# Optimization experiments

Hardware: AMD Instinct MI355X
Metric: run time of the kernel (lower is better)

Reference implementation:

```python
import jax, jax.numpy as jnp
import numpy as np

N, E, G = 10000, 80000, 64
F_IN, D, EA, H = 14, 64, 4, 128


def setup_inputs() -> dict:
    key = jax.random.key(0)
    ks = jax.random.split(key, 16)
    f32 = jnp.float32
    def nrm(k, shape, s=0.1):
        return jax.random.normal(k, shape, f32) * s
    return {
        "x": jax.random.normal(ks[0], (N, F_IN), f32),
        "edge_index": jax.random.randint(ks[1], (2, E), 0, N),
        "edge_attr": jax.random.uniform(ks[2], (E, EA), f32),
        "batch": jnp.sort(jax.random.randint(ks[3], (N,), 0, G)),
        "do_dropout": 0,
        "lin0_w": nrm(ks[4], (F_IN, D)), "lin0_b": jnp.zeros((D,), f32),
        "h1_w": nrm(ks[5], (EA, H)), "h1_b": jnp.zeros((H,), f32),
        "h2_w": nrm(ks[6], (H, D * D), 0.02), "h2_b": jnp.zeros((D * D,), f32),
        "conv_root": nrm(ks[7], (D, D)), "conv_bias": jnp.zeros((D,), f32),
        "gru_w_ih": nrm(ks[8], (3 * D, D)), "gru_w_hh": nrm(ks[9], (3 * D, D)),
        "gru_b_ih": jnp.zeros((3 * D,), f32), "gru_b_hh": jnp.zeros((3 * D,), f32),
        "lstm_w_ih": nrm(ks[10], (4 * D, 2 * D)), "lstm_w_hh": nrm(ks[11], (4 * D, D)),
        "lstm_b_ih": jnp.zeros((4 * D,), f32), "lstm_b_hh": jnp.zeros((4 * D,), f32),
        "lin1_w": nrm(ks[12], (2 * D, D)), "lin1_b": jnp.zeros((D,), f32),
        "lin2_w": nrm(ks[13], (D, 1)), "lin2_b": jnp.zeros((1,), f32),
    }


def _seg_softmax(e, seg, n):
    m = jax.ops.segment_max(e, seg, num_segments=n)
    ex = jnp.exp(e - m[seg])
    s = jax.ops.segment_sum(ex, seg, num_segments=n)
    return ex / s[seg]


def _forward(x, edge_index, edge_attr, batch,
             lin0_w, lin0_b, h1_w, h1_b, h2_w, h2_b, conv_root, conv_bias,
             gru_w_ih, gru_w_hh, gru_b_ih, gru_b_hh,
             lstm_w_ih, lstm_w_hh, lstm_b_ih, lstm_b_hh,
             lin1_w, lin1_b, lin2_w, lin2_b):
    src, tgt = edge_index[0], edge_index[1]
    out = jax.nn.relu(x @ lin0_w + lin0_b)              # [N, D]
    h = out
    # edge-conditioned weights: MLP(edge_attr) -> [E, D, D]
    W_e = (jax.nn.relu(edge_attr @ h1_w + h1_b) @ h2_w + h2_b).reshape(E, D, D)
    deg = jax.ops.segment_sum(jnp.ones((E,), out.dtype), tgt, num_segments=N)
    deg = jnp.maximum(deg, 1.0)[:, None]
    for _ in range(3):
        msg = jnp.einsum("ei,eio->eo", out[src], W_e)   # per-edge matmul
        agg = jax.ops.segment_sum(msg, tgt, num_segments=N) / deg  # mean aggr
        m = jax.nn.relu(agg + out @ conv_root + conv_bias)
        # single GRU step (torch nn.GRU, 1 layer, seq_len=1)
        gi = m @ gru_w_ih.T + gru_b_ih
        gh = h @ gru_w_hh.T + gru_b_hh
        ir, iz, in_ = jnp.split(gi, 3, axis=-1)
        hr, hz, hn = jnp.split(gh, 3, axis=-1)
        r = jax.nn.sigmoid(ir + hr)
        z = jax.nn.sigmoid(iz + hz)
        n = jnp.tanh(in_ + r * hn)
        h = (1.0 - z) * n + z * h
        out = h
    # Set2Set pooling, 3 processing steps
    q_star = jnp.zeros((G, 2 * D), out.dtype)
    hs = jnp.zeros((G, D), out.dtype)
    cs = jnp.zeros((G, D), out.dtype)
    for _ in range(3):
        gates = q_star @ lstm_w_ih.T + lstm_b_ih + hs @ lstm_w_hh.T + lstm_b_hh
        i, f, g, o = jnp.split(gates, 4, axis=-1)
        cs = jax.nn.sigmoid(f) * cs + jax.nn.sigmoid(i) * jnp.tanh(g)
        hs = jax.nn.sigmoid(o) * jnp.tanh(cs)
        q = hs                                          # [G, D]
        e = jnp.sum(out * q[batch], axis=-1)            # [N]
        a = _seg_softmax(e, batch, G)
        r = jax.ops.segment_sum(a[:, None] * out, batch, num_segments=G)
        q_star = jnp.concatenate([q, r], axis=-1)
    y = jax.nn.relu(q_star @ lin1_w + lin1_b)
    # do_dropout=False in this reference (eval mode): dropout is identity
    y = y @ lin2_w + lin2_b
    return y.reshape(-1)


def reference(x, edge_index, edge_attr, batch, do_dropout,
              lin0_w, lin0_b, h1_w, h1_b, h2_w, h2_b, conv_root, conv_bias,
              gru_w_ih, gru_w_hh, gru_b_ih, gru_b_hh,
              lstm_w_ih, lstm_w_hh, lstm_b_ih, lstm_b_hh,
              lin1_w, lin1_b, lin2_w, lin2_b):
    return _forward(x, edge_index, edge_attr, batch,
                    lin0_w, lin0_b, h1_w, h1_b, h2_w, h2_b, conv_root, conv_bias,
                    gru_w_ih, gru_w_hh, gru_b_ih, gru_b_hh,
                    lstm_w_ih, lstm_w_hh, lstm_b_ih, lstm_b_hh,
                    lin1_w, lin1_b, lin2_w, lin2_b)
```

## Files before the change

kernel.cpp:

```cpp
#include <hip/hip_runtime.h>
#include <math.h>

#define N_NODES 10000
#define N_EDGES 80000
#define N_GRAPH 64
#define DD 64
#define HIDW 128
#define F_IN 14
#define EAD 4

typedef _Float16 f16x8 __attribute__((ext_vector_type(8)));
typedef float f32x4 __attribute__((ext_vector_type(4)));

__device__ __forceinline__ float sigmoidf_(float x){ return 1.0f/(1.0f+expf(-x)); }

__global__ __launch_bounds__(256) void k_prep_misc(
    const float* __restrict__ h2w, _Float16* __restrict__ Bp,
    const float* __restrict__ gih, const float* __restrict__ ghh,
    const float* __restrict__ lih, const float* __restrict__ lhh,
    float* __restrict__ WihT, float* __restrict__ WhhT,
    float* __restrict__ IhT,  float* __restrict__ HhT,
    const int* __restrict__ tgt, int* __restrict__ cnt,
    const int* __restrict__ batch, int* __restrict__ goff,
    const float* __restrict__ x, const float* __restrict__ l0w,
    const float* __restrict__ l0b, float* __restrict__ s)
{
  int idx = blockIdx.x*256 + threadIdx.x;
  if (idx < 524288){
    int j = idx & 7, l = (idx >> 3) & 63, cg = (idx >> 9) & 3, st = idx >> 11;
    int k = st*32 + ((l >> 4) << 3) + j;
    int h = k >> 6, i = k & 63, o = cg*16 + (l & 15);
    Bp[idx] = (_Float16)h2w[(size_t)h*4096 + i*64 + o];
    return;
  }
  idx -= 524288;
  if (idx < 12288){ int k=idx/192, j=idx%192; WihT[idx]=gih[j*64+k]; return; }
  idx -= 12288;
  if (idx < 12288){ int k=idx/192, j=idx%192; WhhT[idx]=ghh[j*64+k]; return; }
  idx -= 12288;
  if (idx < 32768){ int k=idx>>8, j=idx&255; IhT[idx]=lih[j*128+k]; return; }
  idx -= 32768;
  if (idx < 16384){ int k=idx>>8, j=idx&255; HhT[idx]=lhh[j*64+k]; return; }
  idx -= 16384;
  if (idx < N_EDGES){ atomicAdd(&cnt[tgt[idx]], 1); return; }
  idx -= N_EDGES;
  if (idx < 65){
    int g = idx, lo = 0, hi = N_NODES;
    while (lo < hi){ int mid = (lo+hi)>>1; if (batch[mid] < g) lo = mid+1; else hi = mid; }
    goff[g] = lo; return;
  }
  idx -= 65;
  if (idx < N_NODES*64){
    int n = idx >> 6, o = idx & 63;
    float acc = l0b[o];
    #pragma unroll
    for (int k=0;k<F_IN;++k) acc += x[n*F_IN + k]*l0w[k*64 + o];
    s[idx] = fmaxf(acc, 0.f);
    return;
  }
}
#define PREP_TOT (524288 + 12288 + 12288 + 32768 + 16384 + N_EDGES + 65 + N_NODES*64)


__global__ __launch_bounds__(1024) void k_scan(const int* __restrict__ cnt, int* __restrict__ offs,
                                               int* __restrict__ cursor, float* __restrict__ deg){
  __shared__ int sc[1024];
  int t = threadIdx.x;
  int base = t*10;
  int loc[10]; int tot = 0;
  #pragma unroll
  for (int j=0;j<10;++j){
    int i = base+j;
    int c = (i < N_NODES) ? cnt[i] : 0;
    loc[j] = tot; tot += c;
  }
  sc[t] = tot; __syncthreads();
  for (int st=1; st<1024; st<<=1){
    int v = (t>=st) ? sc[t-st] : 0;
    __syncthreads();
    sc[t] += v;
    __syncthreads();
  }
  int ex = sc[t] - tot;
  #pragma unroll
  for (int j=0;j<10;++j){
    int i = base+j;
    if (i < N_NODES){
      int o = ex + loc[j];
      offs[i] = o; cursor[i] = o;
      int c = cnt[i];
      deg[i] = (float)(c > 0 ? c : 1);
    }
  }
  if (t == 1023) offs[N_NODES] = sc[1023];
}

__global__ void k_sortE(const int* __restrict__ tgt, const int* __restrict__ src,
                        int* __restrict__ cursor, int* __restrict__ srcS, int* __restrict__ pos){
  int e = blockIdx.x*256 + threadIdx.x;
  if (e < N_EDGES){
    int p = atomicAdd(&cursor[tgt[e]], 1);
    srcS[p] = src[e];
    pos[e] = p;
  }
}

__global__ __launch_bounds__(256) void k_hid(const float* __restrict__ ea,
    const float* __restrict__ h1_w, const float* __restrict__ h1_b,
    const int* __restrict__ pos, _Float16* __restrict__ hidS){
  int tid = threadIdx.x;
  int g = tid >> 7, j = tid & 127;
  __shared__ float eL[2][EAD];
  __shared__ int pL[2];
  if (tid < 8){ int gg = tid>>2, k = tid&3; eL[gg][k] = ea[(blockIdx.x*2+gg)*EAD + k]; }
  if (tid < 2) pL[tid] = pos[blockIdx.x*2 + tid];
  __syncthreads();
  float v = h1_b[j];
  #pragma unroll
  for (int k=0;k<EAD;++k) v += eL[g][k]*h1_w[k*HIDW + j];
  hidS[(size_t)pL[g]*HIDW + j] = (_Float16)fmaxf(v, 0.f);
}

__global__ __launch_bounds__(256) void k_aggpre(
    const float* __restrict__ s, const _Float16* __restrict__ hidS,
    const int* __restrict__ offs, const int* __restrict__ srcS,
    _Float16* __restrict__ P, float* __restrict__ Ssum){
  int t = blockIdx.x;
  int tid = threadIdx.x;
  int i8 = tid & 7, hb = tid >> 3;
  __shared__ float sL[8][64];
  __shared__ float hidT[8][128];
  float acc[4][8];
  #pragma unroll
  for (int r=0;r<4;++r)
    #pragma unroll
    for (int ii=0;ii<8;++ii) acc[r][ii] = 0.f;
  float ss[8];
  #pragma unroll
  for (int ii=0;ii<8;++ii) ss[ii] = 0.f;
  int e0 = offs[t], e1 = offs[t+1];
  for (int base = e0; base < e1; base += 8){
    int ecnt = min(8, e1 - base);
    __syncthreads();
    for (int a = tid; a < ecnt*64; a += 256){
      int j = a >> 6, ii = a & 63;
      sL[j][ii] = s[(size_t)srcS[base+j]*64 + ii];
    }
    for (int a = tid; a < ecnt*128; a += 256){
      int j = a >> 7, hh = a & 127;
      hidT[j][(hh & 3)*32 + (hh >> 2)] = (float)hidS[(size_t)(base+j)*HIDW + hh];
    }
    __syncthreads();
    for (int j=0;j<ecnt;++j){
      float hv[4], sv[8];
      #pragma unroll
      for (int r=0;r<4;++r) hv[r] = hidT[j][r*32 + hb];
      #pragma unroll
      for (int ii=0;ii<8;++ii) sv[ii] = sL[j][i8*8 + ii];
      #pragma unroll
      for (int r=0;r<4;++r)
        #pragma unroll
        for (int ii=0;ii<8;++ii) acc[r][ii] += hv[r]*sv[ii];
      if (hb == 0){
        #pragma unroll
        for (int ii=0;ii<8;++ii) ss[ii] += sv[ii];
      }
    }
  }
  _Float16* row = P + (size_t)t*8192;
  #pragma unroll
  for (int r=0;r<4;++r){
    f16x8 pk;
    #pragma unroll
    for (int ii=0;ii<8;++ii) pk[ii] = (_Float16)acc[r][ii];
    *(f16x8*)(row + (hb*4 + r)*64 + i8*8) = pk;
  }
  if (hb == 0){
    float4 v0 = make_float4(ss[0],ss[1],ss[2],ss[3]);
    float4 v1 = make_float4(ss[4],ss[5],ss[6],ss[7]);
    *(float4*)(Ssum + (size_t)t*64 + i8*8)     = v0;
    *(float4*)(Ssum + (size_t)t*64 + i8*8 + 4) = v1;
  }
}

__global__ __launch_bounds__(256) void k_gemm_fused(
    const _Float16* __restrict__ A, const _Float16* __restrict__ Bp,
    const float* __restrict__ Ssum, const float* __restrict__ h2b,
    const float* __restrict__ deg, float* __restrict__ s,
    const float* __restrict__ conv_root, const float* __restrict__ conv_bias,
    const float* __restrict__ WihT, const float* __restrict__ WhhT,
    const float* __restrict__ bih, const float* __restrict__ bhh)
{
  __shared__ _Float16 tile[2][16*1024];
  __shared__ float aggL[16][68];
  __shared__ float hS[16][64];
  __shared__ float xS[16][68];
  int tid = threadIdx.x;
  int t0 = blockIdx.x*16;
  const size_t rowB = (size_t)8192*2;
  int sub = tid >> 7, colb = (tid & 127)*16;
  const char* Ab = (const char*)A + (size_t)t0*rowB;
  f16x8 rg[8];
  int cg = tid >> 6, lane = tid & 63;
  int row = lane & 15, kb = lane >> 4;
  int swz = (row & 7) << 4;
  f32x4 acc = {0.f,0.f,0.f,0.f};

  #pragma unroll
  for (int i2=0;i2<8;++i2){
    int r = i2*2 + sub;
    rg[i2] = *(const f16x8*)(Ab + (size_t)r*rowB + (size_t)(colb ^ ((r&7)<<4)));
  }
  #pragma unroll
  for (int i2=0;i2<8;++i2){
    int r = i2*2 + sub;
    *(f16x8*)((char*)tile[0] + r*2048 + colb) = rg[i2];
  }
  for (int y = 0; y < 8; ++y){
    if (y < 7){
      #pragma unroll
      for (int i2=0;i2<8;++i2){
        int r = i2*2 + sub;
        rg[i2] = *(const f16x8*)(Ab + (size_t)r*rowB + (size_t)(y+1)*2048 + (size_t)(colb ^ ((r&7)<<4)));
      }
    }
    __syncthreads();
    const char* tb = (const char*)tile[y&1] + row*2048;
    int fr0 = y*128;
    #pragma unroll 8
    for (int st = 0; st < 32; ++st){
      f16x8 af = *(const f16x8*)(tb + ((st*64 + kb*16) ^ swz));
      f16x8 bf = *(const f16x8*)(Bp + ((size_t)(fr0 + st*4 + cg)*64 + lane)*8);
      acc = __builtin_amdgcn_mfma_f32_16x16x32_f16(af, bf, acc, 0, 0, 0);
    }
    if (y < 7){
      #pragma unroll
      for (int i2=0;i2<8;++i2){
        int r = i2*2 + sub;
        *(f16x8*)((char*)tile[(y+1)&1] + r*2048 + colb) = rg[i2];
      }
    }
  }
  #pragma unroll
  for (int r=0;r<4;++r) aggL[kb*4 + r][cg*16 + row] = acc[r];
  for (int a = tid; a < 1024; a += 256){
    int nn = a >> 6, o = a & 63;
    hS[nn][o] = s[(size_t)(t0+nn)*64 + o];
    xS[nn][o] = Ssum[(size_t)(t0+nn)*64 + o];
  }
  __syncthreads();
  int o = tid & 63, ng = tid >> 6;
  float aM[4];
  #pragma unroll
  for (int u=0;u<4;++u) aM[u] = aggL[ng + 4*u][o];
  for (int k=0;k<64;++k){
    float w2 = h2b[k*64 + o];
    #pragma unroll
    for (int u=0;u<4;++u) aM[u] += xS[ng + 4*u][k]*w2;
  }
  #pragma unroll
  for (int u=0;u<4;++u) aM[u] = aM[u]/deg[t0 + ng + 4*u] + conv_bias[o];
  for (int k=0;k<64;++k){
    float cr = conv_root[k*64 + o];
    #pragma unroll
    for (int u=0;u<4;++u) aM[u] += hS[ng + 4*u][k]*cr;
  }
  float mM[4];
  #pragma unroll
  for (int u=0;u<4;++u) mM[u] = fmaxf(aM[u], 0.f);
  __syncthreads();
  #pragma unroll
  for (int u=0;u<4;++u) xS[ng + 4*u][o] = mM[u];
  __syncthreads();
  float gi0[4], gi1[4], gi2[4], gh0[4], gh1[4], gh2[4];
  #pragma unroll
  for (int u=0;u<4;++u){
    gi0[u] = bih[o];     gh0[u] = bhh[o];
    gi1[u] = bih[64+o];  gh1[u] = bhh[64+o];
    gi2[u] = bih[128+o]; gh2[u] = bhh[128+o];
  }
  for (int k=0;k<64;++k){
    float wi0 = WihT[k*192 + o], wi1 = WihT[k*192 + 64 + o], wi2 = WihT[k*192 + 128 + o];
    float wh0 = WhhT[k*192 + o], wh1 = WhhT[k*192 + 64 + o], wh2 = WhhT[k*192 + 128 + o];
    #pragma unroll
    for (int u=0;u<4;++u){
      float mk = xS[ng + 4*u][k], hk = hS[ng + 4*u][k];
      gi0[u] += mk*wi0; gh0[u] += hk*wh0;
      gi1[u] += mk*wi1; gh1[u] += hk*wh1;
      gi2[u] += mk*wi2; gh2[u] += hk*wh2;
    }
  }
  #pragma unroll
  for (int u=0;u<4;++u){
    int nn = ng + 4*u;
    float r = sigmoidf_(gi0[u] + gh0[u]);
    float z = sigmoidf_(gi1[u] + gh1[u]);
    float nv = tanhf(gi2[u] + r*gh2[u]);
    float hnew = (1.f - z)*nv + z*hS[nn][o];
    s[(size_t)(t0+nn)*64 + o] = hnew;
  }
}


__global__ __launch_bounds__(256) void k_s2s_all(const float* __restrict__ sND,
    const int* __restrict__ goff,
    const float* __restrict__ IhT, const float* __restrict__ HhT,
    const float* __restrict__ bih, const float* __restrict__ bhh,
    float* __restrict__ ebuf,
    const float* __restrict__ lin1_w, const float* __restrict__ lin1_b,
    const float* __restrict__ lin2_w, const float* __restrict__ lin2_b,
    float* __restrict__ out)
{
  const int CAP = 256;
  __shared__ float sG[256][68];
  __shared__ float eL[256];
  __shared__ float qL[128], hL[64], cL[64], gate[256];
  __shared__ float red[4], redw[4], red2[4][64];
  int g = blockIdx.x, tid = threadIdx.x;
  int w = tid >> 6, lane = tid & 63;
  int n0 = goff[g], n1 = goff[g+1], cnt = n1 - n0;
  int ncap = cnt < CAP ? cnt : CAP;
  for (int idx = tid; idx < ncap*64; idx += 256)
    sG[idx>>6][idx&63] = sND[(size_t)(n0 + (idx>>6))*64 + (idx&63)];
  if (tid < 128) qL[tid] = 0.f;
  if (tid < 64){ hL[tid] = 0.f; cL[tid] = 0.f; }
  __syncthreads();
  for (int step = 0; step < 3; ++step){
    float acc = bih[tid] + bhh[tid];
    #pragma unroll 8
    for (int k=0;k<128;++k) acc += qL[k]*IhT[k*256 + tid];
    #pragma unroll 8
    for (int k=0;k<64;++k)  acc += hL[k]*HhT[k*256 + tid];
    gate[tid] = acc;
    __syncthreads();
    if (tid < 64){
      float i = sigmoidf_(gate[tid]);
      float f = sigmoidf_(gate[64+tid]);
      float gg = tanhf(gate[128+tid]);
      float o = sigmoidf_(gate[192+tid]);
      float cc = f*cL[tid] + i*gg;
      hL[tid] = o*tanhf(cc);
      cL[tid] = cc;
    }
    __syncthreads();
    float wmax = -INFINITY;
    for (int r = w; r < cnt; r += 4){
      float v = (r < CAP) ? sG[r][lane] : sND[(size_t)(n0+r)*64 + lane];
      float p = v * hL[lane];
      #pragma unroll
      for (int s2=32; s2>0; s2>>=1) p += __shfl_xor(p, s2, 64);
      if (lane == 0){ if (r < CAP) eL[r] = p; else ebuf[n0+r] = p; }
      wmax = fmaxf(wmax, p);
    }
    if (lane == 0) red[w] = wmax;
    __syncthreads();
    float m = fmaxf(fmaxf(red[0], red[1]), fmaxf(red[2], red[3]));
    float racc = 0.f, ws = 0.f;
    for (int r = w; r < cnt; r += 4){
      float e = (r < CAP) ? eL[r] : ebuf[n0+r];
      float a = expf(e - m);
      float v = (r < CAP) ? sG[r][lane] : sND[(size_t)(n0+r)*64 + lane];
      racc += a * v;
      ws += a;
    }
    red2[w][lane] = racc;
    if (lane == 0) redw[w] = ws;
    __syncthreads();
    if (tid < 64){
      float rs = red2[0][lane]+red2[1][lane]+red2[2][lane]+red2[3][lane];
      float st = redw[0]+redw[1]+redw[2]+redw[3];
      float rr = (st > 0.f) ? rs/st : 0.f;
      qL[lane] = hL[lane];
      qL[64+lane] = rr;
    }
    __syncthreads();
  }
  {
    float facc = 0.f;
    for (int k = w*32; k < w*32+32; ++k) facc += qL[k]*lin1_w[k*64 + lane];
    red2[w][lane] = facc;
  }
  __syncthreads();
  if (tid < 64){
    float z = fmaxf(lin1_b[lane] + red2[0][lane]+red2[1][lane]+red2[2][lane]+red2[3][lane], 0.f);
    float p = z * lin2_w[lane];
    #pragma unroll
    for (int s2=32; s2>0; s2>>=1) p += __shfl_xor(p, s2, 64);
    if (lane == 0) out[g] = p + lin2_b[0];
  }
}


static inline size_t alignup(size_t x){ return (x + 255) & ~(size_t)255; }

extern "C" void kernel_launch(void* const* d_in, const int* in_sizes, int n_in,
                              void* d_out, int out_size, void* d_ws, size_t ws_size,
                              hipStream_t stream){
  const float* x      = (const float*)d_in[0];
  const int*   ei     = (const int*)  d_in[1];
  const float* ea     = (const float*)d_in[2];
  const int*   batch  = (const int*)  d_in[3];
  const float* lin0_w = (const float*)d_in[5];
  const float* lin0_b = (const float*)d_in[6];
  const float* h1_w   = (const float*)d_in[7];
  const float* h1_b   = (const float*)d_in[8];
  const float* h2_w   = (const float*)d_in[9];
  const float* h2_b   = (const float*)d_in[10];
  const float* conv_root = (const float*)d_in[11];
  const float* conv_bias = (const float*)d_in[12];
  const float* gru_w_ih  = (const float*)d_in[13];
  const float* gru_w_hh  = (const float*)d_in[14];
  const float* gru_b_ih  = (const float*)d_in[15];
  const float* gru_b_hh  = (const float*)d_in[16];
  const float* lstm_w_ih = (const float*)d_in[17];
  const float* lstm_w_hh = (const float*)d_in[18];
  const float* lstm_b_ih = (const float*)d_in[19];
  const float* lstm_b_hh = (const float*)d_in[20];
  const float* lin1_w = (const float*)d_in[21];
  const float* lin1_b = (const float*)d_in[22];
  const float* lin2_w = (const float*)d_in[23];
  const float* lin2_b = (const float*)d_in[24];
  (void)in_sizes; (void)n_in; (void)out_size; (void)ws_size;

  const int* srcA = ei;
  const int* tgtA = ei + N_EDGES;

  char* p = (char*)d_ws;
  size_t off = 0;
  auto take = [&](size_t bytes)->char*{ char* q = p + off; off = alignup(off + bytes); return q; };
  _Float16* Bpack = (_Float16*)take((size_t)524288*2);
  float* sbuf     = (float*)take((size_t)N_NODES*DD*4);
  float* Ssum     = (float*)take((size_t)N_NODES*DD*4);
  _Float16* hidS  = (_Float16*)take((size_t)N_EDGES*HIDW*2);
  float* WihT    = (float*)take(12288*4);
  float* WhhT    = (float*)take(12288*4);
  float* IhT     = (float*)take(32768*4);
  float* HhT     = (float*)take(16384*4);
  float* deg     = (float*)take(N_NODES*4);
  int*   cnt     = (int*)  take(N_NODES*4);
  int*   offs    = (int*)  take((N_NODES+1)*4);
  int*   cursor  = (int*)  take(N_NODES*4);
  int*   srcS    = (int*)  take(N_EDGES*4);
  int*   pos     = (int*)  take(N_EDGES*4);
  int*   goff    = (int*)  take(65*4);
  float* ebuf    = (float*)take(N_NODES*4);
  _Float16* Pbuf = (_Float16*)take((size_t)N_NODES*8192*2);

  hipMemsetAsync(cnt, 0, N_NODES*4, stream);

  k_prep_misc<<<(PREP_TOT + 255)/256, 256, 0, stream>>>(
      h2_w, Bpack, gru_w_ih, gru_w_hh, lstm_w_ih, lstm_w_hh,
      WihT, WhhT, IhT, HhT, tgtA, cnt, batch, goff, x, lin0_w, lin0_b, sbuf);
  k_scan<<<1, 1024, 0, stream>>>(cnt, offs, cursor, deg);
  k_sortE<<<(N_EDGES+255)/256, 256, 0, stream>>>(tgtA, srcA, cursor, srcS, pos);
  k_hid<<<N_EDGES/2, 256, 0, stream>>>(ea, h1_w, h1_b, pos, hidS);

  for (int it = 0; it < 3; ++it){
    k_aggpre<<<N_NODES, 256, 0, stream>>>(sbuf, hidS, offs, srcS, Pbuf, Ssum);
    k_gemm_fused<<<N_NODES/16, 256, 0, stream>>>(Pbuf, Bpack, Ssum, h2_b, deg, sbuf,
                                                 conv_root, conv_bias, WihT, WhhT,
                                                 gru_b_ih, gru_b_hh);
  }

  k_s2s_all<<<N_GRAPH, 256, 0, stream>>>(sbuf, goff, IhT, HhT, lstm_b_ih, lstm_b_hh, ebuf,
                                         lin1_w, lin1_b, lin2_w, lin2_b, (float*)d_out);
}
```

Before: 666.0 us.

## Chunk node aggregation into two halves with ping-pong state buffers

Splits each message-passing iteration into two node chunks so the per-node P intermediate (8192 fp16 per node) only needs to hold about half the nodes, shrinking the workspace and possibly letting it stay resident in the large last-level cache between the aggregate and GEMM kernels. Node state is now double-buffered (sOld/sNew), since the two chunks otherwise would read state already updated by the other chunk. The GEMM kernel's LDS tile is halved (k-step of 512 instead of 1024, 16 stages) and degree division becomes multiplication by a precomputed reciprocal. It doubles the kernel launches per iteration.

```diff
diff --git a/kernel.cpp b/kernel.cpp
--- a/kernel.cpp
+++ b/kernel.cpp
@@ -63,7 +63,7 @@
 
 
 __global__ __launch_bounds__(1024) void k_scan(const int* __restrict__ cnt, int* __restrict__ offs,
-                                               int* __restrict__ cursor, float* __restrict__ deg){
+                                               int* __restrict__ cursor, float* __restrict__ deginv){
   __shared__ int sc[1024];
   int t = threadIdx.x;
   int base = t*10;
@@ -89,7 +89,7 @@
       int o = ex + loc[j];
       offs[i] = o; cursor[i] = o;
       int c = cnt[i];
-      deg[i] = (float)(c > 0 ? c : 1);
+      deginv[i] = 1.0f/(float)(c > 0 ? c : 1);
     }
   }
   if (t == 1023) offs[N_NODES] = sc[1023];
@@ -124,8 +124,8 @@
 __global__ __launch_bounds__(256) void k_aggpre(
     const float* __restrict__ s, const _Float16* __restrict__ hidS,
     const int* __restrict__ offs, const int* __restrict__ srcS,
-    _Float16* __restrict__ P, float* __restrict__ Ssum){
-  int t = blockIdx.x;
+    _Float16* __restrict__ P, float* __restrict__ Ssum, int n0){
+  int t = n0 + blockIdx.x;
   int tid = threadIdx.x;
   int i8 = tid & 7, hb = tid >> 3;
   __shared__ float sL[8][64];
@@ -167,7 +167,7 @@
       }
     }
   }
-  _Float16* row = P + (size_t)t*8192;
+  _Float16* row = P + (size_t)blockIdx.x*8192;
   #pragma unroll
   for (int r=0;r<4;++r){
     f16x8 pk;
@@ -186,91 +186,92 @@
 __global__ __launch_bounds__(256) void k_gemm_fused(
     const _Float16* __restrict__ A, const _Float16* __restrict__ Bp,
     const float* __restrict__ Ssum, const float* __restrict__ h2b,
-    const float* __restrict__ deg, float* __restrict__ s,
+    const float* __restrict__ deginv, const float* __restrict__ sOld,
+    float* __restrict__ sNew,
     const float* __restrict__ conv_root, const float* __restrict__ conv_bias,
     const float* __restrict__ WihT, const float* __restrict__ WhhT,
-    const float* __restrict__ bih, const float* __restrict__ bhh)
+    const float* __restrict__ bih, const float* __restrict__ bhh, int n0)
 {
-  __shared__ _Float16 tile[2][16*1024];
-  __shared__ float aggL[16][68];
-  __shared__ float hS[16][64];
-  __shared__ float xS[16][68];
+  __shared__ __align__(16) char smem[32768];
   int tid = threadIdx.x;
-  int t0 = blockIdx.x*16;
-  const size_t rowB = (size_t)8192*2;
-  int sub = tid >> 7, colb = (tid & 127)*16;
-  const char* Ab = (const char*)A + (size_t)t0*rowB;
-  f16x8 rg[8];
+  int t0 = n0 + blockIdx.x*16;
+  const char* Ab = (const char*)A + (size_t)blockIdx.x*16*16384;
+  int sub = tid >> 6;
+  int colb = (tid & 63) * 16;
+  f16x8 rg[4];
   int cg = tid >> 6, lane = tid & 63;
   int row = lane & 15, kb = lane >> 4;
   int swz = (row & 7) << 4;
   f32x4 acc = {0.f,0.f,0.f,0.f};
 
   #pragma unroll
-  for (int i2=0;i2<8;++i2){
-    int r = i2*2 + sub;
-    rg[i2] = *(const f16x8*)(Ab + (size_t)r*rowB + (size_t)(colb ^ ((r&7)<<4)));
-  }
-  #pragma unroll
-  for (int i2=0;i2<8;++i2){
-    int r = i2*2 + sub;
-    *(f16x8*)((char*)tile[0] + r*2048 + colb) = rg[i2];
-  }
-  for (int y = 0; y < 8; ++y){
-    if (y < 7){
-      #pragma unroll
-      for (int i2=0;i2<8;++i2){
-        int r = i2*2 + sub;
-        rg[i2] = *(const f16x8*)(Ab + (size_t)r*rowB + (size_t)(y+1)*2048 + (size_t)(colb ^ ((r&7)<<4)));
+  for (int i2=0;i2<4;++i2){
+    int r = i2*4 + sub;
+    rg[i2] = *(const f16x8*)(Ab + (size_t)r*16384 + (size_t)(colb ^ ((r&7)<<4)));
+  }
+  #pragma unroll
+  for (int i2=0;i2<4;++i2){
+    int r = i2*4 + sub;
+    *(f16x8*)(smem + r*1024 + colb) = rg[i2];
+  }
+  for (int y = 0; y < 16; ++y){
+    if (y < 15){
+      #pragma unroll
+      for (int i2=0;i2<4;++i2){
+        int r = i2*4 + sub;
+        rg[i2] = *(const f16x8*)(Ab + (size_t)r*16384 + (size_t)(y+1)*1024 + (size_t)(colb ^ ((r&7)<<4)));
       }
     }
     __syncthreads();
-    const char* tb = (const char*)tile[y&1] + row*2048;
-    int fr0 = y*128;
-    #pragma unroll 8
-    for (int st = 0; st < 32; ++st){
+    const char* tb = smem + (y&1)*16384 + row*1024;
+    #pragma unroll 16
+    for (int st = 0; st < 16; ++st){
       f16x8 af = *(const f16x8*)(tb + ((st*64 + kb*16) ^ swz));
-      f16x8 bf = *(const f16x8*)(Bp + ((size_t)(fr0 + st*4 + cg)*64 + lane)*8);
+      f16x8 bf = *(const f16x8*)(Bp + ((size_t)((y*16 + st)*4 + cg)*64 + lane)*8);
       acc = __builtin_amdgcn_mfma_f32_16x16x32_f16(af, bf, acc, 0, 0, 0);
     }
-    if (y < 7){
-      #pragma unroll
-      for (int i2=0;i2<8;++i2){
-        int r = i2*2 + sub;
-        *(f16x8*)((char*)tile[(y+1)&1] + r*2048 + colb) = rg[i2];
+    if (y < 15){
+      char* tw = smem + ((y+1)&1)*16384;
+      #pragma unroll
+      for (int i2=0;i2<4;++i2){
+        int r = i2*4 + sub;
+        *(f16x8*)(tw + r*1024 + colb) = rg[i2];
       }
     }
   }
-  #pragma unroll
-  for (int r=0;r<4;++r) aggL[kb*4 + r][cg*16 + row] = acc[r];
+  float* aggL = (float*)smem;
+  float* hSs  = (float*)(smem + 4352);
+  float* xSs  = (float*)(smem + 8448);
+  #pragma unroll
+  for (int r=0;r<4;++r) aggL[(kb*4 + r)*68 + cg*16 + row] = acc[r];
   for (int a = tid; a < 1024; a += 256){
-    int nn = a >> 6, o = a & 63;
-    hS[nn][o] = s[(size_t)(t0+nn)*64 + o];
-    xS[nn][o] = Ssum[(size_t)(t0+nn)*64 + o];
+    int nn = a >> 6, o2 = a & 63;
+    hSs[nn*64 + o2] = sOld[(size_t)(t0+nn)*64 + o2];
+    xSs[nn*68 + o2] = Ssum[(size_t)(t0+nn)*64 + o2];
   }
   __syncthreads();
   int o = tid & 63, ng = tid >> 6;
   float aM[4];
   #pragma unroll
-  for (int u=0;u<4;++u) aM[u] = aggL[ng + 4*u][o];
+  for (int u=0;u<4;++u) aM[u] = aggL[(ng + 4*u)*68 + o];
   for (int k=0;k<64;++k){
     float w2 = h2b[k*64 + o];
     #pragma unroll
-    for (int u=0;u<4;++u) aM[u] += xS[ng + 4*u][k]*w2;
-  }
-  #pragma unroll
-  for (int u=0;u<4;++u) aM[u] = aM[u]/deg[t0 + ng + 4*u] + conv_bias[o];
+    for (int u=0;u<4;++u) aM[u] += xSs[(ng + 4*u)*68 + k]*w2;
+  }
+  #pragma unroll
+  for (int u=0;u<4;++u) aM[u] = aM[u]*deginv[t0 + ng + 4*u] + conv_bias[o];
   for (int k=0;k<64;++k){
     float cr = conv_root[k*64 + o];
     #pragma unroll
-    for (int u=0;u<4;++u) aM[u] += hS[ng + 4*u][k]*cr;
+    for (int u=0;u<4;++u) aM[u] += hSs[(ng + 4*u)*64 + k]*cr;
   }
   float mM[4];
   #pragma unroll
   for (int u=0;u<4;++u) mM[u] = fmaxf(aM[u], 0.f);
   __syncthreads();
   #pragma unroll
-  for (int u=0;u<4;++u) xS[ng + 4*u][o] = mM[u];
+  for (int u=0;u<4;++u) xSs[(ng + 4*u)*68 + o] = mM[u];
   __syncthreads();
   float gi0[4], gi1[4], gi2[4], gh0[4], gh1[4], gh2[4];
   #pragma unroll
@@ -284,7 +285,7 @@
     float wh0 = WhhT[k*192 + o], wh1 = WhhT[k*192 + 64 + o], wh2 = WhhT[k*192 + 128 + o];
     #pragma unroll
     for (int u=0;u<4;++u){
-      float mk = xS[ng + 4*u][k], hk = hS[ng + 4*u][k];
+      float mk = xSs[(ng + 4*u)*68 + k], hk = hSs[(ng + 4*u)*64 + k];
       gi0[u] += mk*wi0; gh0[u] += hk*wh0;
       gi1[u] += mk*wi1; gh1[u] += hk*wh1;
       gi2[u] += mk*wi2; gh2[u] += hk*wh2;
@@ -296,8 +297,8 @@
     float r = sigmoidf_(gi0[u] + gh0[u]);
     float z = sigmoidf_(gi1[u] + gh1[u]);
     float nv = tanhf(gi2[u] + r*gh2[u]);
-    float hnew = (1.f - z)*nv + z*hS[nn][o];
-    s[(size_t)(t0+nn)*64 + o] = hnew;
+    float hnew = (1.f - z)*nv + z*hSs[nn*64 + o];
+    sNew[(size_t)(t0+nn)*64 + o] = hnew;
   }
 }
 
@@ -429,14 +430,15 @@
   size_t off = 0;
   auto take = [&](size_t bytes)->char*{ char* q = p + off; off = alignup(off + bytes); return q; };
   _Float16* Bpack = (_Float16*)take((size_t)524288*2);
-  float* sbuf     = (float*)take((size_t)N_NODES*DD*4);
+  float* sbufA    = (float*)take((size_t)N_NODES*DD*4);
+  float* sbufB    = (float*)take((size_t)N_NODES*DD*4);
   float* Ssum     = (float*)take((size_t)N_NODES*DD*4);
   _Float16* hidS  = (_Float16*)take((size_t)N_EDGES*HIDW*2);
   float* WihT    = (float*)take(12288*4);
   float* WhhT    = (float*)take(12288*4);
   float* IhT     = (float*)take(32768*4);
   float* HhT     = (float*)take(16384*4);
-  float* deg     = (float*)take(N_NODES*4);
+  float* deginv  = (float*)take(N_NODES*4);
   int*   cnt     = (int*)  take(N_NODES*4);
   int*   offs    = (int*)  take((N_NODES+1)*4);
   int*   cursor  = (int*)  take(N_NODES*4);
@@ -444,24 +446,31 @@
   int*   pos     = (int*)  take(N_EDGES*4);
   int*   goff    = (int*)  take(65*4);
   float* ebuf    = (float*)take(N_NODES*4);
-  _Float16* Pbuf = (_Float16*)take((size_t)N_NODES*8192*2);
+  _Float16* Pbuf = (_Float16*)take((size_t)5008*8192*2);
 
   hipMemsetAsync(cnt, 0, N_NODES*4, stream);
 
   k_prep_misc<<<(PREP_TOT + 255)/256, 256, 0, stream>>>(
       h2_w, Bpack, gru_w_ih, gru_w_hh, lstm_w_ih, lstm_w_hh,
-      WihT, WhhT, IhT, HhT, tgtA, cnt, batch, goff, x, lin0_w, lin0_b, sbuf);
-  k_scan<<<1, 1024, 0, stream>>>(cnt, offs, cursor, deg);
+      WihT, WhhT, IhT, HhT, tgtA, cnt, batch, goff, x, lin0_w, lin0_b, sbufA);
+  k_scan<<<1, 1024, 0, stream>>>(cnt, offs, cursor, deginv);
   k_sortE<<<(N_EDGES+255)/256, 256, 0, stream>>>(tgtA, srcA, cursor, srcS, pos);
   k_hid<<<N_EDGES/2, 256, 0, stream>>>(ea, h1_w, h1_b, pos, hidS);
 
+  float* sCur = sbufA;
+  float* sNxt = sbufB;
+  const int cb[3] = {0, 4992, 10000};
   for (int it = 0; it < 3; ++it){
-    k_aggpre<<<N_NODES, 256, 0, stream>>>(sbuf, hidS, offs, srcS, Pbuf, Ssum);
-    k_gemm_fused<<<N_NODES/16, 256, 0, stream>>>(Pbuf, Bpack, Ssum, h2_b, deg, sbuf,
-                                                 conv_root, conv_bias, WihT, WhhT,
-                                                 gru_b_ih, gru_b_hh);
-  }
-
-  k_s2s_all<<<N_GRAPH, 256, 0, stream>>>(sbuf, goff, IhT, HhT, lstm_b_ih, lstm_b_hh, ebuf,
+    for (int c = 0; c < 2; ++c){
+      int nn0 = cb[c], ncnt = cb[c+1] - nn0;
+      k_aggpre<<<ncnt, 256, 0, stream>>>(sCur, hidS, offs, srcS, Pbuf, Ssum, nn0);
+      k_gemm_fused<<<ncnt/16, 256, 0, stream>>>(Pbuf, Bpack, Ssum, h2_b, deginv, sCur, sNxt,
+                                                conv_root, conv_bias, WihT, WhhT,
+                                                gru_b_ih, gru_b_hh, nn0);
+    }
+    float* tmp = sCur; sCur = sNxt; sNxt = tmp;
+  }
+
+  k_s2s_all<<<N_GRAPH, 256, 0, stream>>>(sCur, goff, IhT, HhT, lstm_b_ih, lstm_b_hh, ebuf,
                                          lin1_w, lin1_b, lin2_w, lin2_b, (float*)d_out);
 }
```

Result: slower. 922.4 us (+38.5%).
